# Optimization experiments

Measured on AMD Instinct MI355X. Metric: run time of the kernel, lower is better.

The kernel has to match this reference:

```python
import jax, jax.numpy as jnp
import numpy as np

DIM = 192
QK_DIM = 192
WIN_S = 8
TOPK = 4


def setup_inputs() -> dict:
    key = jax.random.key(0)
    k1, k2, k3 = jax.random.split(key, 3)
    x = jax.random.normal(k1, (2, DIM, 256, 256), dtype=jnp.float32)
    # torch Linear default init ~ U(-1/sqrt(in), 1/sqrt(in)); scaled normal is fine as stand-in
    w_qkv = jax.random.normal(k2, (DIM, QK_DIM + QK_DIM + DIM), dtype=jnp.float32) * (DIM ** -0.5)
    b_qkv = jax.random.normal(k3, (QK_DIM + QK_DIM + DIM,), dtype=jnp.float32) * 0.01
    return {"x": x, "w_qkv": w_qkv, "b_qkv": b_qkv}


def reference(x, w_qkv, b_qkv):
    b, c, h, w = x.shape
    n_h, n_w = h // WIN_S, w // WIN_S
    hs, ws = h // n_h, w // n_w  # == WIN_S
    n_hw = n_h * n_w
    s_hw = hs * ws

    # b c h w -> b (n_h n_w) hs ws c
    xw = x.transpose(0, 2, 3, 1)                      # b h w c
    xw = xw.reshape(b, n_h, hs, n_w, ws, c)
    xw = xw.transpose(0, 1, 3, 2, 4, 5).reshape(b, n_hw, hs, ws, c)

    # QKVLinear: dim -> qk_dim + (qk_dim + dim)
    qkv = jnp.einsum('bnhwc,cd->bnhwd', xw, w_qkv) + b_qkv
    q = qkv[..., :QK_DIM]                             # (b, n_hw, hs, ws, qk_dim)
    kv = qkv[..., QK_DIM:]                            # (b, n_hw, hs, ws, qk_dim+dim)

    # WinProj 'mean'
    q_win = q.mean(axis=(2, 3))                       # (b, n_hw, qk_dim)
    k_win = kv[..., :QK_DIM].mean(axis=(2, 3))        # (b, n_hw, qk_dim)

    # TopkRouting (diff_routing=False -> detached; forward math identical)
    scale = QK_DIM ** -0.5
    logits = jnp.einsum('bnc,bmc->bnm', q_win * scale, k_win)  # (b, n_hw, n_hw)
    topk_logit, topk_idx = jax.lax.top_k(logits, TOPK)         # (b, n_hw, topk)
    r_weight = jax.nn.softmax(topk_logit, axis=-1)             # unused (mul_weight='none')

    # KVGather (mul_weight='none'): gather full kv pixel blocks of selected windows
    kv_pix = kv.reshape(b, n_hw, s_hw, QK_DIM + DIM)
    kv_pix_sel = jax.vmap(lambda kvb, idx: kvb[idx])(kv_pix, topk_idx)  # (b, n_hw, topk, s_hw, qk_dim+dim)

    v_pix_sel = kv_pix_sel[..., QK_DIM:]              # (b, n_hw, topk, s_hw, dim)
    return v_pix_sel
```

## Files before the change

kernel.cpp:

```cpp
#include <hip/hip_runtime.h>
#include <hip/hip_bf16.h>
#include <math.h>

#define NB   2
#define NC   192
#define HW   256
#define NWIN 1024
#define SHW  64
#define NDQ  192
#define WCOL 576

typedef short bf16x8 __attribute__((ext_vector_type(8)));
typedef float f32x4  __attribute__((ext_vector_type(4)));

__device__ inline unsigned int bf16pack(float a, float b) {
  unsigned int ua = __builtin_bit_cast(unsigned int, a);
  ua += 0x7fffu + ((ua >> 16) & 1u);
  unsigned int ub = __builtin_bit_cast(unsigned int, b);
  ub += 0x7fffu + ((ub >> 16) & 1u);
  return (ua >> 16) | (ub & 0xffff0000u);
}

__device__ inline unsigned short bf16r(float a) {
  unsigned int ua = __builtin_bit_cast(unsigned int, a);
  ua += 0x7fffu + ((ua >> 16) & 1u);
  return (unsigned short)(ua >> 16);
}

__global__ __launch_bounds__(256) void k0_wvt(const float* __restrict__ w,
                                              unsigned short* __restrict__ wvt) {
  int id = blockIdx.x * 256 + threadIdx.x;
  int d = id / NC, c = id - d * NC;
  wvt[d * NC + c] = bf16r(w[c * WCOL + 2 * NDQ + d]);
}

__global__ __launch_bounds__(1024) void kA_vgemm(const float* __restrict__ x,
                                                 const unsigned short* __restrict__ wvt,
                                                 const float* __restrict__ w,
                                                 const float* __restrict__ bias,
                                                 unsigned int* __restrict__ vtmp,
                                                 float* __restrict__ qw,
                                                 float* __restrict__ kwT) {
  int b = blockIdx.y, g = blockIdx.x;
  int m0 = g * 4;
  int wh = m0 >> 5, ww0 = m0 & 31;
  int t = threadIdx.x;

  __shared__ unsigned short Xs[16384];
  __shared__ float part[32][65];
  __shared__ float xmLds[4][NC];

  int L = t & 63, wv = t >> 6;
  int win = wv >> 2, dq = wv & 3;
  int col = L & 15, kg = L >> 4;

  f32x4 acc[4][3];
#pragma unroll
  for (int dt = 0; dt < 3; ++dt) {
    float bv = bias[2 * NDQ + dq * 48 + dt * 16 + col];
    f32x4 bi = {bv, bv, bv, bv};
#pragma unroll
    for (int pt = 0; pt < 4; ++pt) acc[pt][dt] = bi;
  }

  int cp = t & 15, gi = t >> 4;
  int r = gi >> 3, w4 = gi & 7;
  int winS = w4 >> 1;
  int pS = r * 8 + (w4 & 1) * 4;
  const float* xb = x + (size_t)(b * NC) * (HW * HW) + (size_t)(wh * 8 + r) * HW + ww0 * 8 + w4 * 4;

  int rw = (t >> 5) & 3, rc = t & 31;

  for (int cc = 0; cc < 6; ++cc) {
    const float* pl = xb + (size_t)(cc * 32 + cp * 2) * (HW * HW);
    float4 va = *(const float4*)pl;
    float4 vb = *(const float4*)(pl + HW * HW);
    float fa[4] = {va.x, va.y, va.z, va.w};
    float fb[4] = {vb.x, vb.y, vb.z, vb.w};
#pragma unroll
    for (int i = 0; i < 4; ++i) {
      int p = pS + i;
      unsigned int pk = bf16pack(fa[i], fb[i]);
      *(unsigned int*)((char*)Xs + (winS * 8192 + p * 128 + ((cp * 4) ^ ((p & 7) << 4)))) = pk;
    }
    part[cp * 2][gi]     = fa[0] + fa[1] + fa[2] + fa[3];
    part[cp * 2 + 1][gi] = fb[0] + fb[1] + fb[2] + fb[3];
    __syncthreads();

    if (t < 128) {
      float s = 0.0f;
#pragma unroll
      for (int rr = 0; rr < 8; ++rr) {
        s += part[rc][rr * 8 + 2 * rw];
        s += part[rc][rr * 8 + 2 * rw + 1];
      }
      xmLds[rw][cc * 32 + rc] = s * (1.0f / 64.0f);
    }

    bf16x8 Bf[3];
#pragma unroll
    for (int dt = 0; dt < 3; ++dt)
      Bf[dt] = *(const bf16x8*)(wvt + (size_t)(dq * 48 + dt * 16 + col) * NC + cc * 32 + kg * 8);

#pragma unroll
    for (int pt = 0; pt < 4; ++pt) {
      int p = pt * 16 + col;
      bf16x8 Af = *(const bf16x8*)((const char*)Xs +
                    (win * 8192 + p * 128 + ((kg * 16) ^ ((p & 7) << 4))));
      acc[pt][0] = __builtin_amdgcn_mfma_f32_16x16x32_bf16(Af, Bf[0], acc[pt][0], 0, 0, 0);
      acc[pt][1] = __builtin_amdgcn_mfma_f32_16x16x32_bf16(Af, Bf[1], acc[pt][1], 0, 0, 0);
      acc[pt][2] = __builtin_amdgcn_mfma_f32_16x16x32_bf16(Af, Bf[2], acc[pt][2], 0, 0, 0);
    }
    __syncthreads();
  }

  unsigned int* vt = vtmp + (size_t)(b * NWIN + m0 + win) * 6144;
#pragma unroll
  for (int pt = 0; pt < 4; ++pt) {
#pragma unroll
    for (int dt = 0; dt < 3; ++dt) {
#pragma unroll
      for (int rrp = 0; rrp < 2; ++rrp) {
        unsigned int pk = bf16pack(acc[pt][dt][rrp * 2], acc[pt][dt][rrp * 2 + 1]);
        vt[(size_t)((((dq * 4 + pt) * 3 + dt) * 2 + rrp) * 64 + L)] = pk;
      }
    }
  }

  for (int o = t; o < 1536; o += 1024) {
    int winq = o / 384;
    int d = o - winq * 384;
    const float* xr = xmLds[winq];
    double a = 0.0;
    for (int c = 0; c < NC; ++c)
      a += (double)xr[c] * (double)w[c * WCOL + d];
    float bv = bias[d];
    int n = m0 + winq;
    if (d < NDQ) {
      float qv = (float)a + bv;
      qw[(size_t)(b * NWIN + n) * NC + d] = qv * 0.0721687836487032f;
    } else {
      float kv = (float)a + bv;
      kwT[(size_t)b * NC * NWIN + (size_t)(d - NDQ) * NWIN + n] = kv;
    }
  }
}

__global__ __launch_bounds__(1024) void k3_topk(const float* __restrict__ qw,
                                                const float* __restrict__ kwT,
                                                int* __restrict__ topk) {
  int b = blockIdx.y, n0 = blockIdx.x * 8;
  int t = threadIdx.x;
  __shared__ float qs[8][NC];
  __shared__ float lg[8][NWIN];
  for (int l = t; l < 8 * NC; l += 1024) {
    int r = l / NC, c = l - r * NC;
    qs[r][c] = qw[(size_t)(b * NWIN + n0 + r) * NC + c];
  }
  __syncthreads();

  int col2 = (t & 511) * 2;
  int rg = (t >> 9) * 4;

  double acc[4][2];
#pragma unroll
  for (int r = 0; r < 4; ++r) { acc[r][0] = 0.0; acc[r][1] = 0.0; }

  const float* kb = kwT + (size_t)b * NC * NWIN;
#pragma unroll 2
  for (int c = 0; c < NC; ++c) {
    float2 kv = *(const float2*)(kb + (size_t)c * NWIN + col2);
    double k0 = (double)kv.x, k1 = (double)kv.y;
#pragma unroll
    for (int r = 0; r < 4; ++r) {
      double q = (double)qs[rg + r][c];
      acc[r][0] += q * k0;
      acc[r][1] += q * k1;
    }
  }
#pragma unroll
  for (int r = 0; r < 4; ++r) {
    lg[rg + r][col2]     = (float)acc[r][0];
    lg[rg + r][col2 + 1] = (float)acc[r][1];
  }
  __syncthreads();

  int wave = t >> 6, lane = t & 63;
  if (wave < 8) {
    int r = wave;
    float v4[4];
    int   i4[4];
#pragma unroll
    for (int j = 0; j < 4; ++j) { v4[j] = -INFINITY; i4[j] = 0x7fffffff; }
    for (int i = 0; i < 16; ++i) {
      int idx = i * 64 + lane;
      float v = lg[r][idx];
      if (v > v4[3] || (v == v4[3] && idx < i4[3])) {
        v4[3] = v; i4[3] = idx;
#pragma unroll
        for (int j = 3; j > 0; --j) {
          if (v4[j] > v4[j-1] || (v4[j] == v4[j-1] && i4[j] < i4[j-1])) {
            float tv = v4[j]; v4[j] = v4[j-1]; v4[j-1] = tv;
            int ti = i4[j]; i4[j] = i4[j-1]; i4[j-1] = ti;
          }
        }
      }
    }
    for (int m = 1; m < 64; m <<= 1) {
      float ov[4]; int oi[4];
#pragma unroll
      for (int j = 0; j < 4; ++j) { ov[j] = __shfl_xor(v4[j], m); oi[j] = __shfl_xor(i4[j], m); }
      float nv[4]; int ni[4];
      int ia = 0, ib = 0;
#pragma unroll
      for (int j = 0; j < 4; ++j) {
        bool ta = (v4[ia] > ov[ib]) || (v4[ia] == ov[ib] && i4[ia] < oi[ib]);
        if (ta) { nv[j] = v4[ia]; ni[j] = i4[ia]; ++ia; }
        else    { nv[j] = ov[ib]; ni[j] = oi[ib]; ++ib; }
      }
#pragma unroll
      for (int j = 0; j < 4; ++j) { v4[j] = nv[j]; i4[j] = ni[j]; }
    }
    if (lane == 0) {
      int n = n0 + r;
#pragma unroll
      for (int k = 0; k < 4; ++k)
        topk[(size_t)(b * NWIN + n) * 4 + k] = i4[k];
    }
  }
}

__global__ __launch_bounds__(512) void kB_gather(const unsigned int* __restrict__ vtmp,
                                                 const int* __restrict__ topk,
                                                 float* __restrict__ out) {
  int id = blockIdx.x;
  int b = id >> 12;
  int m = topk[id];
  const unsigned int* src = vtmp + (size_t)(b * NWIN + m) * 6144;
  float* dst = out + (size_t)id * (SHW * NC);
  int t = threadIdx.x;
#pragma unroll
  for (int i = 0; i < 3; ++i) {
    int u = i * 512 + t;
    int j    = u & 15;
    int rem  = u >> 4;
    int rrp  = rem & 1;
    int rem2 = rem >> 1;
    int dt = rem2 % 3;
    int qp = rem2 / 3;
    int pt = qp & 3, dq = qp >> 2;
    uint4 v = *(const uint4*)(src + (size_t)rem * 64 + j * 4);
    int p0 = pt * 16 + (j >> 2) * 4 + rrp * 2;
    int d0 = dq * 48 + dt * 16 + (j & 3) * 4;
    float4 plo, phi;
    plo.x = __builtin_bit_cast(float, v.x << 16);
    phi.x = __builtin_bit_cast(float, v.x & 0xffff0000u);
    plo.y = __builtin_bit_cast(float, v.y << 16);
    phi.y = __builtin_bit_cast(float, v.y & 0xffff0000u);
    plo.z = __builtin_bit_cast(float, v.z << 16);
    phi.z = __builtin_bit_cast(float, v.z & 0xffff0000u);
    plo.w = __builtin_bit_cast(float, v.w << 16);
    phi.w = __builtin_bit_cast(float, v.w & 0xffff0000u);
    *(float4*)(dst + (size_t)p0 * NC + d0)       = plo;
    *(float4*)(dst + (size_t)(p0 + 1) * NC + d0) = phi;
  }
}

extern "C" void kernel_launch(void* const* d_in, const int* in_sizes, int n_in,
                              void* d_out, int out_size, void* d_ws, size_t ws_size,
                              hipStream_t stream) {
  const float* x    = (const float*)d_in[0];
  const float* w    = (const float*)d_in[1];
  const float* bias = (const float*)d_in[2];
  float* out = (float*)d_out;

  unsigned int* vtmp = (unsigned int*)d_ws;
  float* qw    = (float*)(vtmp + (size_t)12582912);
  float* kwT   = qw + 393216;
  int*   topk  = (int*)(kwT + 393216);
  unsigned short* wvt = (unsigned short*)(topk + 8192);

  k0_wvt<<<144, 256, 0, stream>>>(w, wvt);
  kA_vgemm<<<dim3(256, 2), 1024, 0, stream>>>(x, wvt, w, bias, vtmp, qw, kwT);
  k3_topk<<<dim3(128, 2), 1024, 0, stream>>>(qw, kwT, topk);
  kB_gather<<<8192, 512, 0, stream>>>(vtmp, topk, out);
}
```

Measured before the change: 232.2 us.

## Split V-GEMM kernel into one window per 256-thread block

Each block of kA_vgemm now handles one window with 256 threads instead of four windows with 1024 threads, giving 2048 blocks. LDS per block shrinks accordingly, and the window-mean q/k projection is restructured so each thread computes both the q and k dot products for one channel. The aim is better occupancy and load balance and less idle time in the serial double-precision projection tail. In exchange the weight tiles are reloaded four times as often, since they are no longer shared across four windows per block.

```diff
diff --git a/kernel.cpp b/kernel.cpp
--- a/kernel.cpp
+++ b/kernel.cpp
@@ -34,24 +34,22 @@
   wvt[d * NC + c] = bf16r(w[c * WCOL + 2 * NDQ + d]);
 }
 
-__global__ __launch_bounds__(1024) void kA_vgemm(const float* __restrict__ x,
-                                                 const unsigned short* __restrict__ wvt,
-                                                 const float* __restrict__ w,
-                                                 const float* __restrict__ bias,
-                                                 unsigned int* __restrict__ vtmp,
-                                                 float* __restrict__ qw,
-                                                 float* __restrict__ kwT) {
-  int b = blockIdx.y, g = blockIdx.x;
-  int m0 = g * 4;
-  int wh = m0 >> 5, ww0 = m0 & 31;
+__global__ __launch_bounds__(256) void kA_vgemm(const float* __restrict__ x,
+                                                const unsigned short* __restrict__ wvt,
+                                                const float* __restrict__ w,
+                                                const float* __restrict__ bias,
+                                                unsigned int* __restrict__ vtmp,
+                                                float* __restrict__ qw,
+                                                float* __restrict__ kwT) {
+  int b = blockIdx.y, m = blockIdx.x;
+  int wh = m >> 5, ww = m & 31;
   int t = threadIdx.x;
 
-  __shared__ unsigned short Xs[16384];
-  __shared__ float part[32][65];
-  __shared__ float xmLds[4][NC];
-
-  int L = t & 63, wv = t >> 6;
-  int win = wv >> 2, dq = wv & 3;
+  __shared__ unsigned short Xs[4096];
+  __shared__ float part[32][17];
+  __shared__ float xmLds[NC];
+
+  int L = t & 63, dq = t >> 6;
   int col = L & 15, kg = L >> 4;
 
   f32x4 acc[4][3];
@@ -64,12 +62,9 @@
   }
 
   int cp = t & 15, gi = t >> 4;
-  int r = gi >> 3, w4 = gi & 7;
-  int winS = w4 >> 1;
-  int pS = r * 8 + (w4 & 1) * 4;
-  const float* xb = x + (size_t)(b * NC) * (HW * HW) + (size_t)(wh * 8 + r) * HW + ww0 * 8 + w4 * 4;
-
-  int rw = (t >> 5) & 3, rc = t & 31;
+  int r = gi >> 1, c4 = gi & 1;
+  int pS = r * 8 + c4 * 4;
+  const float* xb = x + (size_t)(b * NC) * (HW * HW) + (size_t)(wh * 8 + r) * HW + ww * 8 + c4 * 4;
 
   for (int cc = 0; cc < 6; ++cc) {
     const float* pl = xb + (size_t)(cc * 32 + cp * 2) * (HW * HW);
@@ -81,20 +76,20 @@
     for (int i = 0; i < 4; ++i) {
       int p = pS + i;
       unsigned int pk = bf16pack(fa[i], fb[i]);
-      *(unsigned int*)((char*)Xs + (winS * 8192 + p * 128 + ((cp * 4) ^ ((p & 7) << 4)))) = pk;
+      *(unsigned int*)((char*)Xs + (p * 128 + ((cp * 4) ^ ((p & 7) << 4)))) = pk;
     }
     part[cp * 2][gi]     = fa[0] + fa[1] + fa[2] + fa[3];
     part[cp * 2 + 1][gi] = fb[0] + fb[1] + fb[2] + fb[3];
     __syncthreads();
 
-    if (t < 128) {
+    if (t < 32) {
       float s = 0.0f;
 #pragma unroll
       for (int rr = 0; rr < 8; ++rr) {
-        s += part[rc][rr * 8 + 2 * rw];
-        s += part[rc][rr * 8 + 2 * rw + 1];
-      }
-      xmLds[rw][cc * 32 + rc] = s * (1.0f / 64.0f);
+        s += part[t][rr * 2];
+        s += part[t][rr * 2 + 1];
+      }
+      xmLds[cc * 32 + t] = s * (1.0f / 64.0f);
     }
 
     bf16x8 Bf[3];
@@ -106,7 +101,7 @@
     for (int pt = 0; pt < 4; ++pt) {
       int p = pt * 16 + col;
       bf16x8 Af = *(const bf16x8*)((const char*)Xs +
-                    (win * 8192 + p * 128 + ((kg * 16) ^ ((p & 7) << 4))));
+                    (p * 128 + ((kg * 16) ^ ((p & 7) << 4))));
       acc[pt][0] = __builtin_amdgcn_mfma_f32_16x16x32_bf16(Af, Bf[0], acc[pt][0], 0, 0, 0);
       acc[pt][1] = __builtin_amdgcn_mfma_f32_16x16x32_bf16(Af, Bf[1], acc[pt][1], 0, 0, 0);
       acc[pt][2] = __builtin_amdgcn_mfma_f32_16x16x32_bf16(Af, Bf[2], acc[pt][2], 0, 0, 0);
@@ -114,7 +109,7 @@
     __syncthreads();
   }
 
-  unsigned int* vt = vtmp + (size_t)(b * NWIN + m0 + win) * 6144;
+  unsigned int* vt = vtmp + (size_t)(b * NWIN + m) * 6144;
 #pragma unroll
   for (int pt = 0; pt < 4; ++pt) {
 #pragma unroll
@@ -127,22 +122,15 @@
     }
   }
 
-  for (int o = t; o < 1536; o += 1024) {
-    int winq = o / 384;
-    int d = o - winq * 384;
-    const float* xr = xmLds[winq];
-    double a = 0.0;
-    for (int c = 0; c < NC; ++c)
-      a += (double)xr[c] * (double)w[c * WCOL + d];
-    float bv = bias[d];
-    int n = m0 + winq;
-    if (d < NDQ) {
-      float qv = (float)a + bv;
-      qw[(size_t)(b * NWIN + n) * NC + d] = qv * 0.0721687836487032f;
-    } else {
-      float kv = (float)a + bv;
-      kwT[(size_t)b * NC * NWIN + (size_t)(d - NDQ) * NWIN + n] = kv;
-    }
+  if (t < NDQ) {
+    double aq = 0.0, ak = 0.0;
+    for (int c = 0; c < NC; ++c) {
+      double xc = (double)xmLds[c];
+      aq += xc * (double)w[c * WCOL + t];
+      ak += xc * (double)w[c * WCOL + NDQ + t];
+    }
+    qw[(size_t)(b * NWIN + m) * NC + t] = ((float)aq + bias[t]) * 0.0721687836487032f;
+    kwT[(size_t)b * NC * NWIN + (size_t)t * NWIN + m] = (float)ak + bias[NDQ + t];
   }
 }
 
@@ -281,7 +269,7 @@
   unsigned short* wvt = (unsigned short*)(topk + 8192);
 
   k0_wvt<<<144, 256, 0, stream>>>(w, wvt);
-  kA_vgemm<<<dim3(256, 2), 1024, 0, stream>>>(x, wvt, w, bias, vtmp, qw, kwT);
+  kA_vgemm<<<dim3(1024, 2), 256, 0, stream>>>(x, wvt, w, bias, vtmp, qw, kwT);
   k3_topk<<<dim3(128, 2), 1024, 0, stream>>>(qw, kwT, topk);
   kB_gather<<<8192, 512, 0, stream>>>(vtmp, topk, out);
 }
```

After: 247.8 us. +6.7%, slower.

## Double-buffer LDS tiles and prefetch next channel chunk in V GEMM

Applied to the files above, without the earlier changes.

The V-projection kernel now double-buffers the shared-memory X tile and partial-sum array, and issues the global loads for the next channel chunk before the MFMA work on the current one. This drops one barrier per iteration and lets global memory latency overlap with compute. In exchange, shared memory use roughly doubles (about 32KB more), which can lower occupancy for the 1024-thread block, and more registers are live for the prefetched values.

```diff
diff --git a/kernel.cpp b/kernel.cpp
--- a/kernel.cpp
+++ b/kernel.cpp
@@ -46,8 +46,8 @@
   int wh = m0 >> 5, ww0 = m0 & 31;
   int t = threadIdx.x;
 
-  __shared__ unsigned short Xs[16384];
-  __shared__ float part[32][65];
+  __shared__ unsigned short Xs[2][16384];
+  __shared__ float part[2][32][65];
   __shared__ float xmLds[4][NC];
 
   int L = t & 63, wv = t >> 6;
@@ -71,28 +71,40 @@
 
   int rw = (t >> 5) & 3, rc = t & 31;
 
+  float4 va, vb;
+  {
+    const float* pl = xb + (size_t)(cp * 2) * (HW * HW);
+    va = *(const float4*)pl;
+    vb = *(const float4*)(pl + HW * HW);
+  }
+
   for (int cc = 0; cc < 6; ++cc) {
-    const float* pl = xb + (size_t)(cc * 32 + cp * 2) * (HW * HW);
-    float4 va = *(const float4*)pl;
-    float4 vb = *(const float4*)(pl + HW * HW);
+    int buf = cc & 1;
     float fa[4] = {va.x, va.y, va.z, va.w};
     float fb[4] = {vb.x, vb.y, vb.z, vb.w};
 #pragma unroll
     for (int i = 0; i < 4; ++i) {
       int p = pS + i;
       unsigned int pk = bf16pack(fa[i], fb[i]);
-      *(unsigned int*)((char*)Xs + (winS * 8192 + p * 128 + ((cp * 4) ^ ((p & 7) << 4)))) = pk;
-    }
-    part[cp * 2][gi]     = fa[0] + fa[1] + fa[2] + fa[3];
-    part[cp * 2 + 1][gi] = fb[0] + fb[1] + fb[2] + fb[3];
+      *(unsigned int*)((char*)Xs[buf] + (winS * 8192 + p * 128 + ((cp * 4) ^ ((p & 7) << 4)))) = pk;
+    }
+    part[buf][cp * 2][gi]     = fa[0] + fa[1] + fa[2] + fa[3];
+    part[buf][cp * 2 + 1][gi] = fb[0] + fb[1] + fb[2] + fb[3];
     __syncthreads();
+
+    float4 nva, nvb;
+    if (cc < 5) {
+      const float* pl = xb + (size_t)((cc + 1) * 32 + cp * 2) * (HW * HW);
+      nva = *(const float4*)pl;
+      nvb = *(const float4*)(pl + HW * HW);
+    }
 
     if (t < 128) {
       float s = 0.0f;
 #pragma unroll
       for (int rr = 0; rr < 8; ++rr) {
-        s += part[rc][rr * 8 + 2 * rw];
-        s += part[rc][rr * 8 + 2 * rw + 1];
+        s += part[buf][rc][rr * 8 + 2 * rw];
+        s += part[buf][rc][rr * 8 + 2 * rw + 1];
       }
       xmLds[rw][cc * 32 + rc] = s * (1.0f / 64.0f);
     }
@@ -105,14 +117,17 @@
 #pragma unroll
     for (int pt = 0; pt < 4; ++pt) {
       int p = pt * 16 + col;
-      bf16x8 Af = *(const bf16x8*)((const char*)Xs +
+      bf16x8 Af = *(const bf16x8*)((const char*)Xs[buf] +
                     (win * 8192 + p * 128 + ((kg * 16) ^ ((p & 7) << 4))));
       acc[pt][0] = __builtin_amdgcn_mfma_f32_16x16x32_bf16(Af, Bf[0], acc[pt][0], 0, 0, 0);
       acc[pt][1] = __builtin_amdgcn_mfma_f32_16x16x32_bf16(Af, Bf[1], acc[pt][1], 0, 0, 0);
       acc[pt][2] = __builtin_amdgcn_mfma_f32_16x16x32_bf16(Af, Bf[2], acc[pt][2], 0, 0, 0);
     }
-    __syncthreads();
-  }
+
+    va = nva; vb = nvb;
+  }
+
+  __syncthreads();
 
   unsigned int* vt = vtmp + (size_t)(b * NWIN + m0 + win) * 6144;
 #pragma unroll
```

Measured after the change: 235.3 us. Within noise of the previous version (+1.4%).
